# Optimization experiments

Hardware: AMD Instinct MI355X
Metric: run time of the kernel (lower is better)

Reference implementation:

```python
import jax, jax.numpy as jnp
import numpy as np

N = 50000       # nodes
E = 800000      # directed edges (avg degree 16)
DIN, DH, DOUT = 128, 128, 64
NUM_LAYERS = 5


def setup_inputs() -> dict:
    key = jax.random.key(0)
    ks = jax.random.split(key, 2 + 2 * NUM_LAYERS)
    x = jax.random.normal(ks[0], (N, DIN), dtype=jnp.float32)
    edge_index = jax.random.randint(ks[1], (2, E), 0, N, dtype=jnp.int64)
    dims = [(DIN, DH)] + [(DH, DH)] * (NUM_LAYERS - 2) + [(DH, DOUT)]
    inp = {"x": x, "edge_index": edge_index}
    for i, (di, do) in enumerate(dims):
        # PyG Linear weight is [out, in]; glorot-ish scale
        inp[f"W{i}"] = jax.random.normal(ks[2 + 2 * i], (do, di), dtype=jnp.float32) / np.sqrt(di)
        inp[f"b{i}"] = jnp.zeros((do,), dtype=jnp.float32)
    return inp


def gcn_conv(x, W, b, src, dst, n):
    """PyG GCNConv: symmetric normalization with self-loops (already appended)."""
    h = x @ W.T                                   # [N, do]
    ones = jnp.ones(src.shape[0], dtype=h.dtype)
    deg = jax.ops.segment_sum(ones, dst, num_segments=n)          # [N]
    dinv = jnp.where(deg > 0, jax.lax.rsqrt(jnp.maximum(deg, 1.0)), 0.0)
    norm = dinv[src] * dinv[dst]                  # [E+N]
    msg = h[src] * norm[:, None]                  # [E+N, do] gather
    out = jax.ops.segment_sum(msg, dst, num_segments=n)           # scatter-add
    return out + b


def reference(x, edge_index, W0, b0, W1, b1, W2, b2, W3, b3, W4, b4):
    n = x.shape[0]
    loop = jnp.arange(n, dtype=edge_index.dtype)
    src = jnp.concatenate([edge_index[0], loop])  # add self-loops
    dst = jnp.concatenate([edge_index[1], loop])
    Ws = [W0, W1, W2, W3, W4]
    bs = [b0, b1, b2, b3, b4]
    for i in range(NUM_LAYERS):
        x = gcn_conv(x, Ws[i], bs[i], src, dst, n)
        if i != NUM_LAYERS - 1:
            x = jax.nn.relu(x)
            # dropout is identity in eval mode (training=False)
    return x
```

## Files before the change

kernel.cpp:

```cpp
#include <hip/hip_runtime.h>
#include <hip/hip_fp16.h>
#include <math.h>


typedef _Float16 f16x8 __attribute__((ext_vector_type(8)));
typedef float f32x4 __attribute__((ext_vector_type(4)));

#define NBIN 128
#define NB 512
#define WCAP 12288


__device__ __forceinline__ int edge_at(const void* ei, int is64, long long idx) {
  if (is64) return (int)((const long long*)ei)[idx];
  return ((const int*)ei)[idx];
}

__device__ __forceinline__ int detect_is64(const int* ei32, int E, int* ldsflag, int tid) {
  if (tid == 0) *ldsflag = 0;
  __syncthreads();
  int lim = (E < 256) ? E : 256;
  if (tid < lim) {
    if (ei32[2 * tid + 1] != 0) atomicOr(ldsflag, 1);
  }
  __syncthreads();
  return (*ldsflag == 0) ? 1 : 0;
}

__global__ __launch_bounds__(512) void k_cnt2(const void* __restrict__ ei, int* __restrict__ bcnt,
                                              int E, int n, int W) {
  __shared__ int cnt[NBIN];
  __shared__ int f64;
  int t = threadIdx.x;
  int is64 = detect_is64((const int*)ei, E, &f64, t);
  if (t < NBIN) cnt[t] = 0;
  __syncthreads();
  int chunk = (E + NB - 1) / NB;
  int base = blockIdx.x * chunk;
  int end = base + chunk;
  if (end > E) end = E;
  for (int i = base + t; i < end; i += 512) {
    int s = edge_at(ei, is64, i);
    int v = edge_at(ei, is64, (long long)E + i);
    if ((unsigned)v < (unsigned)n && (unsigned)s < (unsigned)n) atomicAdd(&cnt[v / W], 1);
  }
  __syncthreads();
  if (t < NBIN) bcnt[blockIdx.x * NBIN + t] = cnt[t];
}

__global__ __launch_bounds__(256) void k_scanb(int* __restrict__ bcnt, int* __restrict__ bintot) {
  __shared__ int buf[NB];
  int bin = blockIdx.x;
  int t = threadIdx.x;
  int a0 = bcnt[(size_t)t * NBIN + bin];
  int a1 = bcnt[(size_t)(t + 256) * NBIN + bin];
  buf[t] = a0;
  buf[t + 256] = a1;
  __syncthreads();
  for (int off = 1; off < NB; off <<= 1) {
    int x0 = (t >= off) ? buf[t - off] : 0;
    int x1 = (t + 256 >= off) ? buf[t + 256 - off] : 0;
    __syncthreads();
    buf[t] += x0;
    buf[t + 256] += x1;
    __syncthreads();
  }
  bcnt[(size_t)t * NBIN + bin] = buf[t] - a0;
  bcnt[(size_t)(t + 256) * NBIN + bin] = buf[t + 256] - a1;
  if (t == 255) bintot[bin] = buf[NB - 1];
}

__global__ __launch_bounds__(512) void k_scat(const void* __restrict__ ei, const int* __restrict__ bintot,
                                              const int* __restrict__ bcnt, uint2* __restrict__ ebin,
                                              int E, int n, int W) {
  __shared__ int f64;
  __shared__ int sb[NBIN];
  __shared__ int cur[NBIN];
  int t = threadIdx.x;
  int is64 = detect_is64((const int*)ei, E, &f64, t);
  if (t < NBIN) sb[t] = bintot[t];
  __syncthreads();
  for (int off = 1; off < NBIN; off <<= 1) {
    int x = 0;
    if (t < NBIN && t >= off) x = sb[t - off];
    __syncthreads();
    if (t < NBIN) sb[t] += x;
    __syncthreads();
  }
  if (t < NBIN) cur[t] = sb[t] - bintot[t] + bcnt[blockIdx.x * NBIN + t];
  __syncthreads();
  int chunk = (E + NB - 1) / NB;
  int base = blockIdx.x * chunk;
  int end = base + chunk;
  if (end > E) end = E;
  for (int i = base + t; i < end; i += 512) {
    int s = edge_at(ei, is64, i);
    int v = edge_at(ei, is64, (long long)E + i);
    if ((unsigned)v < (unsigned)n && (unsigned)s < (unsigned)n) {
      int pos = atomicAdd(&cur[v / W], 1);
      ebin[pos] = make_uint2((unsigned)s, (unsigned)v);
    }
  }
}

__global__ __launch_bounds__(256) void k_build(const uint2* __restrict__ ebin, const int* __restrict__ bintot,
                                               int* __restrict__ row_ptr, float* __restrict__ dinv,
                                               int* __restrict__ col, int n, int W) {
  __shared__ int hist[512];
  __shared__ int scanBuf[512];
  __shared__ int sb[NBIN];
  __shared__ unsigned int win[WCAP];
  int t = threadIdx.x;
  int b = blockIdx.x;
  if (t < NBIN) sb[t] = bintot[t];
  __syncthreads();
  for (int off = 1; off < NBIN; off <<= 1) {
    int x = 0;
    if (t < NBIN && t >= off) x = sb[t - off];
    __syncthreads();
    if (t < NBIN) sb[t] += x;
    __syncthreads();
  }
  int ebase = sb[b] - bintot[b];
  int ecnt = bintot[b];
  int etotal = sb[NBIN - 1];

  int v0 = b * W;
  int v1 = v0 + W;
  if (v1 > n) v1 = n;
  int nloc = v1 - v0;
  if (nloc <= 0) {
    if (b == NBIN - 1 && t == 0) row_ptr[n] = etotal;
    return;
  }

  for (int i = t; i < 512; i += 256) { hist[i] = 0; scanBuf[i] = 0; }
  __syncthreads();
  for (int j = t; j < ecnt; j += 256) {
    uint2 e = ebin[ebase + j];
    atomicAdd(&hist[(int)e.y - v0], 1);
  }
  __syncthreads();
  for (int i = t; i < nloc; i += 256) {
    scanBuf[i] = hist[i];
    dinv[v0 + i] = 1.0f / sqrtf((float)(hist[i] + 1));
  }
  __syncthreads();
  int i1 = t, i2 = t + 256;
  for (int off = 1; off < 512; off <<= 1) {
    int a = (i1 >= off) ? scanBuf[i1 - off] : 0;
    int c = (i2 >= off) ? scanBuf[i2 - off] : 0;
    __syncthreads();
    scanBuf[i1] += a;
    scanBuf[i2] += c;
    __syncthreads();
  }
  for (int i = t; i < nloc; i += 256) row_ptr[v0 + i] = ebase + scanBuf[i] - hist[i];
  if (b == NBIN - 1 && t == 0) row_ptr[n] = etotal;
  __syncthreads();
  for (int i = t; i < nloc; i += 256) hist[i] = scanBuf[i] - hist[i];
  __syncthreads();
  if (ecnt <= WCAP) {
    for (int j = t; j < ecnt; j += 256) {
      uint2 e = ebin[ebase + j];
      int pos = atomicAdd(&hist[(int)e.y - v0], 1);
      win[pos] = e.x;
    }
    __syncthreads();
    for (int j = t; j < ecnt; j += 256) col[ebase + j] = (int)win[j];
  } else {
    for (int j = t; j < ecnt; j += 256) {
      uint2 e = ebin[ebase + j];
      int pos = atomicAdd(&hist[(int)e.y - v0], 1);
      col[ebase + pos] = (int)e.x;
    }
  }
}


__global__ __launch_bounds__(256) void k_split_x(const float* __restrict__ X, unsigned int* __restrict__ Xh,
                                                 unsigned int* __restrict__ Xr, int n2) {
  int i = blockIdx.x * 256 + threadIdx.x;
  if (i >= n2) return;
  float2 v = ((const float2*)X)[i];
  __half hx = __float2half(v.x), hy = __float2half(v.y);
  float rx = v.x - __half2float(hx), ry = v.y - __half2float(hy);
  __half rxh = __float2half(rx), ryh = __float2half(ry);
  Xh[i] = ((unsigned int)*(unsigned short*)&hy << 16) | *(unsigned short*)&hx;
  Xr[i] = ((unsigned int)*(unsigned short*)&ryh << 16) | *(unsigned short*)&rxh;
}

__global__ __launch_bounds__(256) void k_split_wall(const float* __restrict__ W0, const float* __restrict__ W1,
                                                    const float* __restrict__ W2, const float* __restrict__ W3,
                                                    const float* __restrict__ W4, unsigned short* __restrict__ Wh,
                                                    unsigned short* __restrict__ Wr, int total) {
  int i = blockIdx.x * 256 + threadIdx.x;
  if (i >= total) return;
  const float* src;
  int off;
  if (i < 65536) {
    int l = i >> 14;
    off = i & 16383;
    src = (l == 0) ? W0 : (l == 1) ? W1 : (l == 2) ? W2 : W3;
  } else {
    off = i - 65536;
    src = W4;
  }
  float v = src[off];
  __half h = __float2half(v);
  float r = v - __half2float(h);
  __half rh = __float2half(r);
  Wh[i] = *(unsigned short*)&h;
  Wr[i] = *(unsigned short*)&rh;
}


template <int DO>
__global__ __launch_bounds__(256) void gemm_mfma(const unsigned short* __restrict__ Xh,
                                                 const unsigned short* __restrict__ Xr,
                                                 const unsigned short* __restrict__ Wh,
                                                 const unsigned short* __restrict__ Wr,
                                                 const float* __restrict__ dinv, __half* __restrict__ G, int n) {
  constexpr int NCG = DO / 16;
  __shared__ unsigned short sWh[DO * 128];
  __shared__ unsigned short sWr[DO * 128];
  const int tid = threadIdx.x;

#pragma unroll
  for (int it = 0; it < DO / 16; ++it) {
    int t = it * 256 + tid;
    int row = t >> 4, ch = t & 15;
    int sch = ch ^ (row & 7);
    const uint4* gh = (const uint4*)&Wh[(size_t)t * 8];
    const uint4* gr = (const uint4*)&Wr[(size_t)t * 8];
    *(uint4*)&sWh[row * 128 + sch * 8] = *gh;
    *(uint4*)&sWr[row * 128 + sch * 8] = *gr;
  }

  const int wv = tid >> 6;
  const int l = tid & 63;
  const int m = l & 15;
  const int ks = l >> 4;
  const int gr0 = blockIdx.x * 64 + wv * 16;
  const int arow = gr0 + m;

  f16x8 ah[4], ar[4];
  const f16x8 z8 = {0, 0, 0, 0, 0, 0, 0, 0};
#pragma unroll
  for (int kb = 0; kb < 4; ++kb) {
    int koff = kb * 32 + ks * 8;
    if (arow < n) {
      ah[kb] = *(const f16x8*)&Xh[(size_t)arow * 128 + koff];
      ar[kb] = *(const f16x8*)&Xr[(size_t)arow * 128 + koff];
    } else {
      ah[kb] = z8;
      ar[kb] = z8;
    }
  }

  f32x4 acc[NCG];
#pragma unroll
  for (int c = 0; c < NCG; ++c) acc[c] = {0.f, 0.f, 0.f, 0.f};

  __syncthreads();

#pragma unroll
  for (int kb = 0; kb < 4; ++kb) {
    int ch = (kb * 4 + ks) ^ (m & 7);
#pragma unroll
    for (int c = 0; c < NCG; ++c) {
      int brow = c * 16 + m;
      f16x8 bh = *(const f16x8*)&sWh[brow * 128 + ch * 8];
      f16x8 br = *(const f16x8*)&sWr[brow * 128 + ch * 8];
      acc[c] = __builtin_amdgcn_mfma_f32_16x16x32_f16(ah[kb], bh, acc[c], 0, 0, 0);
      acc[c] = __builtin_amdgcn_mfma_f32_16x16x32_f16(ah[kb], br, acc[c], 0, 0, 0);
      acc[c] = __builtin_amdgcn_mfma_f32_16x16x32_f16(ar[kb], bh, acc[c], 0, 0, 0);
    }
  }

  int r0 = gr0 + ks * 4;
  float dv[4];
#pragma unroll
  for (int i = 0; i < 4; ++i) dv[i] = (r0 + i < n) ? dinv[r0 + i] : 0.f;
#pragma unroll
  for (int c = 0; c < NCG; ++c) {
#pragma unroll
    for (int i = 0; i < 4; ++i) {
      int row = r0 + i;
      if (row < n) G[(size_t)row * DO + c * 16 + m] = __float2half(dv[i] * acc[c][i]);
    }
  }
}


__device__ __forceinline__ float2 h2f(unsigned int u) {
  __half2 h = *(__half2*)&u;
  return __half22float2(h);
}

__global__ __launch_bounds__(256) void aggregate128(const unsigned int* __restrict__ G, const float* __restrict__ dinv,
                                                    const float* __restrict__ bias, const int* __restrict__ rp,
                                                    const int* __restrict__ col, unsigned int* __restrict__ Yh,
                                                    unsigned int* __restrict__ Yr, int n) {
  int v = (int)((blockIdx.x * 256 + threadIdx.x) >> 6);
  int lane = threadIdx.x & 63;
  if (v >= n) return;
  int s = rp[v], e = rp[v + 1];
  float2 a0 = h2f(G[(size_t)v * 64 + lane]);
  float2 a1 = make_float2(0.f, 0.f), a2 = make_float2(0.f, 0.f), a3 = make_float2(0.f, 0.f);
  float2 a4 = make_float2(0.f, 0.f), a5 = make_float2(0.f, 0.f);
  float2 a6 = make_float2(0.f, 0.f), a7 = make_float2(0.f, 0.f);
  int t = s;
  while (t < e) {
    int batch = e - t;
    if (batch > 64) batch = 64;
    int ci = col[t + (lane < batch ? lane : batch - 1)];
    int j = 0;
    for (; j + 8 <= batch; j += 8) {
      int u0 = __shfl(ci, j, 64), u1 = __shfl(ci, j + 1, 64);
      int u2 = __shfl(ci, j + 2, 64), u3 = __shfl(ci, j + 3, 64);
      int u4 = __shfl(ci, j + 4, 64), u5 = __shfl(ci, j + 5, 64);
      int u6 = __shfl(ci, j + 6, 64), u7 = __shfl(ci, j + 7, 64);
      unsigned int g0 = G[(size_t)u0 * 64 + lane];
      unsigned int g1 = G[(size_t)u1 * 64 + lane];
      unsigned int g2 = G[(size_t)u2 * 64 + lane];
      unsigned int g3 = G[(size_t)u3 * 64 + lane];
      unsigned int g4 = G[(size_t)u4 * 64 + lane];
      unsigned int g5 = G[(size_t)u5 * 64 + lane];
      unsigned int g6 = G[(size_t)u6 * 64 + lane];
      unsigned int g7 = G[(size_t)u7 * 64 + lane];
      float2 f0 = h2f(g0), f1 = h2f(g1), f2 = h2f(g2), f3 = h2f(g3);
      float2 f4 = h2f(g4), f5 = h2f(g5), f6 = h2f(g6), f7 = h2f(g7);
      a0.x += f0.x; a0.y += f0.y;
      a1.x += f1.x; a1.y += f1.y;
      a2.x += f2.x; a2.y += f2.y;
      a3.x += f3.x; a3.y += f3.y;
      a4.x += f4.x; a4.y += f4.y;
      a5.x += f5.x; a5.y += f5.y;
      a6.x += f6.x; a6.y += f6.y;
      a7.x += f7.x; a7.y += f7.y;
    }
    for (; j < batch; ++j) {
      int u = __shfl(ci, j, 64);
      float2 f = h2f(G[(size_t)u * 64 + lane]);
      a0.x += f.x; a0.y += f.y;
    }
    t += batch;
  }
  float sx = ((a0.x + a1.x) + (a2.x + a3.x)) + ((a4.x + a5.x) + (a6.x + a7.x));
  float sy = ((a0.y + a1.y) + (a2.y + a3.y)) + ((a4.y + a5.y) + (a6.y + a7.y));
  float dv = dinv[v];
  float2 bb = ((const float2*)bias)[lane];
  float ox = fmaxf(fmaf(dv, sx, bb.x), 0.f);
  float oy = fmaxf(fmaf(dv, sy, bb.y), 0.f);
  __half hx = __float2half(ox), hy = __float2half(oy);
  float rx = ox - __half2float(hx), ry = oy - __half2float(hy);
  __half rxh = __float2half(rx), ryh = __float2half(ry);
  size_t o = (size_t)v * 64 + lane;
  Yh[o] = ((unsigned int)*(unsigned short*)&hy << 16) | *(unsigned short*)&hx;
  Yr[o] = ((unsigned int)*(unsigned short*)&ryh << 16) | *(unsigned short*)&rxh;
}

__global__ __launch_bounds__(256) void aggregate64(const unsigned short* __restrict__ G, const float* __restrict__ dinv,
                                                   const float* __restrict__ bias, const int* __restrict__ rp,
                                                   const int* __restrict__ col, float* __restrict__ Y, int n) {
  int v = (int)((blockIdx.x * 256 + threadIdx.x) >> 6);
  int lane = threadIdx.x & 63;
  if (v >= n) return;
  int s = rp[v], e = rp[v + 1];
  float a0 = __half2float(*(const __half*)&G[(size_t)v * 64 + lane]);
  float a1 = 0.f, a2 = 0.f, a3 = 0.f;
  float a4 = 0.f, a5 = 0.f, a6 = 0.f, a7 = 0.f;
  int t = s;
  while (t < e) {
    int batch = e - t;
    if (batch > 64) batch = 64;
    int ci = col[t + (lane < batch ? lane : batch - 1)];
    int j = 0;
    for (; j + 8 <= batch; j += 8) {
      int u0 = __shfl(ci, j, 64), u1 = __shfl(ci, j + 1, 64);
      int u2 = __shfl(ci, j + 2, 64), u3 = __shfl(ci, j + 3, 64);
      int u4 = __shfl(ci, j + 4, 64), u5 = __shfl(ci, j + 5, 64);
      int u6 = __shfl(ci, j + 6, 64), u7 = __shfl(ci, j + 7, 64);
      unsigned short g0 = G[(size_t)u0 * 64 + lane];
      unsigned short g1 = G[(size_t)u1 * 64 + lane];
      unsigned short g2 = G[(size_t)u2 * 64 + lane];
      unsigned short g3 = G[(size_t)u3 * 64 + lane];
      unsigned short g4 = G[(size_t)u4 * 64 + lane];
      unsigned short g5 = G[(size_t)u5 * 64 + lane];
      unsigned short g6 = G[(size_t)u6 * 64 + lane];
      unsigned short g7 = G[(size_t)u7 * 64 + lane];
      a0 += __half2float(*(const __half*)&g0);
      a1 += __half2float(*(const __half*)&g1);
      a2 += __half2float(*(const __half*)&g2);
      a3 += __half2float(*(const __half*)&g3);
      a4 += __half2float(*(const __half*)&g4);
      a5 += __half2float(*(const __half*)&g5);
      a6 += __half2float(*(const __half*)&g6);
      a7 += __half2float(*(const __half*)&g7);
    }
    for (; j < batch; ++j) {
      int u = __shfl(ci, j, 64);
      unsigned short g = G[(size_t)u * 64 + lane];
      a0 += __half2float(*(const __half*)&g);
    }
    t += batch;
  }
  float sum = ((a0 + a1) + (a2 + a3)) + ((a4 + a5) + (a6 + a7));
  Y[(size_t)v * 64 + lane] = fmaf(dinv[v], sum, bias[lane]);
}


extern "C" void kernel_launch(void* const* d_in, const int* in_sizes, int n_in,
                              void* d_out, int out_size, void* d_ws, size_t ws_size,
                              hipStream_t stream) {
  const float* x = (const float*)d_in[0];
  const void* ei = d_in[1];
  const int N = in_sizes[0] / 128;
  const int E = in_sizes[1] / 2;
  const float* W[5] = {(const float*)d_in[2], (const float*)d_in[4], (const float*)d_in[6],
                       (const float*)d_in[8], (const float*)d_in[10]};
  const float* B[5] = {(const float*)d_in[3], (const float*)d_in[5], (const float*)d_in[7],
                       (const float*)d_in[9], (const float*)d_in[11]};
  const int Wbin = (N + NBIN - 1) / NBIN;

  char* p = (char*)d_ws;
  unsigned short* xyh = (unsigned short*)p;  p += (size_t)N * 128 * 2;
  unsigned short* xyr = (unsigned short*)p;  p += (size_t)N * 128 * 2;
  __half* g = (__half*)p;                    p += (size_t)N * 128 * 2;
  uint2* ebin = (uint2*)g;
  unsigned short* wh = (unsigned short*)p;   p += (size_t)5 * 16384 * 2;
  unsigned short* wr = (unsigned short*)p;   p += (size_t)5 * 16384 * 2;
  float* dinv = (float*)p;                   p += (size_t)N * 4;
  int* col = (int*)p;                        p += (size_t)E * 4;
  int* row_ptr = (int*)p;                    p += (size_t)(N + 1) * 4;
  int* bcnt = (int*)p;                       p += (size_t)NB * NBIN * 4;
  int* bintot = (int*)p;                     p += NBIN * 4;

  k_cnt2<<<NB, 512, 0, stream>>>(ei, bcnt, E, N, Wbin);
  k_scanb<<<NBIN, 256, 0, stream>>>(bcnt, bintot);
  k_scat<<<NB, 512, 0, stream>>>(ei, bintot, bcnt, ebin, E, N, Wbin);
  k_build<<<NBIN, 256, 0, stream>>>(ebin, bintot, row_ptr, dinv, col, N, Wbin);

  k_split_x<<<(N * 64 + 255) / 256, 256, 0, stream>>>(x, (unsigned int*)xyh, (unsigned int*)xyr, N * 64);
  k_split_wall<<<(73728 + 255) / 256, 256, 0, stream>>>(W[0], W[1], W[2], W[3], W[4], wh, wr, 73728);

  const int gb = (N + 63) / 64;
  const int ab = (N * 64 + 255) / 256;

  for (int l = 0; l < 4; ++l) {
    gemm_mfma<128><<<gb, 256, 0, stream>>>(xyh, xyr, wh + l * 16384, wr + l * 16384, dinv, g, N);
    aggregate128<<<ab, 256, 0, stream>>>((const unsigned int*)g, dinv, B[l], row_ptr, col,
                                         (unsigned int*)xyh, (unsigned int*)xyr, N);
  }
  gemm_mfma<64><<<gb, 256, 0, stream>>>(xyh, xyr, wh + 4 * 16384, wr + 4 * 16384, dinv, g, N);
  aggregate64<<<ab, 256, 0, stream>>>((const unsigned short*)g, dinv, B[4], row_ptr, col, (float*)d_out, N);
}
```

Baseline: 303.2 us.

## Fuse neighbor aggregation with next layer's MFMA GEMM via LDS staging

Replaces the separate aggregate128 and gemm_mfma launches for the middle layers with one kernel. A block aggregates 64 nodes into split fp16 hi/lo tiles held in LDS, then multiplies them by the next layer's weights with MFMA and writes the scaled result to a ping-pong buffer. This is meant to remove the global write and re-read of the intermediate activations and cut the number of launches. In exchange the aggregation runs only 4 waves per block over 16 rows each, with LDS pressure that may limit occupancy and latency hiding for the gathers.

```diff
diff --git a/kernel.cpp b/kernel.cpp
--- a/kernel.cpp
+++ b/kernel.cpp
@@ -9,6 +9,7 @@
 #define NBIN 128
 #define NB 512
 #define WCAP 12288
+#define SXW 136
 
 
 __device__ __forceinline__ int edge_at(const void* ei, int is64, long long idx) {
@@ -298,68 +299,132 @@
   return __half22float2(h);
 }
 
-__global__ __launch_bounds__(256) void aggregate128(const unsigned int* __restrict__ G, const float* __restrict__ dinv,
-                                                    const float* __restrict__ bias, const int* __restrict__ rp,
-                                                    const int* __restrict__ col, unsigned int* __restrict__ Yh,
-                                                    unsigned int* __restrict__ Yr, int n) {
-  int v = (int)((blockIdx.x * 256 + threadIdx.x) >> 6);
-  int lane = threadIdx.x & 63;
-  if (v >= n) return;
-  int s = rp[v], e = rp[v + 1];
-  float2 a0 = h2f(G[(size_t)v * 64 + lane]);
-  float2 a1 = make_float2(0.f, 0.f), a2 = make_float2(0.f, 0.f), a3 = make_float2(0.f, 0.f);
-  float2 a4 = make_float2(0.f, 0.f), a5 = make_float2(0.f, 0.f);
-  float2 a6 = make_float2(0.f, 0.f), a7 = make_float2(0.f, 0.f);
-  int t = s;
-  while (t < e) {
-    int batch = e - t;
-    if (batch > 64) batch = 64;
-    int ci = col[t + (lane < batch ? lane : batch - 1)];
-    int j = 0;
-    for (; j + 8 <= batch; j += 8) {
-      int u0 = __shfl(ci, j, 64), u1 = __shfl(ci, j + 1, 64);
-      int u2 = __shfl(ci, j + 2, 64), u3 = __shfl(ci, j + 3, 64);
-      int u4 = __shfl(ci, j + 4, 64), u5 = __shfl(ci, j + 5, 64);
-      int u6 = __shfl(ci, j + 6, 64), u7 = __shfl(ci, j + 7, 64);
-      unsigned int g0 = G[(size_t)u0 * 64 + lane];
-      unsigned int g1 = G[(size_t)u1 * 64 + lane];
-      unsigned int g2 = G[(size_t)u2 * 64 + lane];
-      unsigned int g3 = G[(size_t)u3 * 64 + lane];
-      unsigned int g4 = G[(size_t)u4 * 64 + lane];
-      unsigned int g5 = G[(size_t)u5 * 64 + lane];
-      unsigned int g6 = G[(size_t)u6 * 64 + lane];
-      unsigned int g7 = G[(size_t)u7 * 64 + lane];
-      float2 f0 = h2f(g0), f1 = h2f(g1), f2 = h2f(g2), f3 = h2f(g3);
-      float2 f4 = h2f(g4), f5 = h2f(g5), f6 = h2f(g6), f7 = h2f(g7);
-      a0.x += f0.x; a0.y += f0.y;
-      a1.x += f1.x; a1.y += f1.y;
-      a2.x += f2.x; a2.y += f2.y;
-      a3.x += f3.x; a3.y += f3.y;
-      a4.x += f4.x; a4.y += f4.y;
-      a5.x += f5.x; a5.y += f5.y;
-      a6.x += f6.x; a6.y += f6.y;
-      a7.x += f7.x; a7.y += f7.y;
-    }
-    for (; j < batch; ++j) {
-      int u = __shfl(ci, j, 64);
-      float2 f = h2f(G[(size_t)u * 64 + lane]);
-      a0.x += f.x; a0.y += f.y;
-    }
-    t += batch;
-  }
-  float sx = ((a0.x + a1.x) + (a2.x + a3.x)) + ((a4.x + a5.x) + (a6.x + a7.x));
-  float sy = ((a0.y + a1.y) + (a2.y + a3.y)) + ((a4.y + a5.y) + (a6.y + a7.y));
-  float dv = dinv[v];
-  float2 bb = ((const float2*)bias)[lane];
-  float ox = fmaxf(fmaf(dv, sx, bb.x), 0.f);
-  float oy = fmaxf(fmaf(dv, sy, bb.y), 0.f);
-  __half hx = __float2half(ox), hy = __float2half(oy);
-  float rx = ox - __half2float(hx), ry = oy - __half2float(hy);
-  __half rxh = __float2half(rx), ryh = __float2half(ry);
-  size_t o = (size_t)v * 64 + lane;
-  Yh[o] = ((unsigned int)*(unsigned short*)&hy << 16) | *(unsigned short*)&hx;
-  Yr[o] = ((unsigned int)*(unsigned short*)&ryh << 16) | *(unsigned short*)&rxh;
-}
+template <int DO>
+__global__ __launch_bounds__(256, 4) void fused_ag(const unsigned int* __restrict__ Gin,
+                                                   const float* __restrict__ dinv,
+                                                   const float* __restrict__ bias,
+                                                   const int* __restrict__ rp, const int* __restrict__ col,
+                                                   const unsigned short* __restrict__ Wh,
+                                                   const unsigned short* __restrict__ Wr,
+                                                   __half* __restrict__ Gout, int n) {
+  constexpr int NCG = DO / 16;
+  __shared__ unsigned short sXh[64 * SXW];
+  __shared__ unsigned short sXr[64 * SXW];
+
+  const int tid = threadIdx.x;
+  const int wv = tid >> 6, lane = tid & 63;
+  const int node0 = blockIdx.x * 64;
+
+  for (int k = 0; k < 16; ++k) {
+    int row = wv * 16 + k;
+    int v = node0 + row;
+    unsigned int ph = 0, pr = 0;
+    if (v < n) {
+      int s = rp[v], e = rp[v + 1];
+      float2 a0 = h2f(Gin[(size_t)v * 64 + lane]);
+      float2 a1 = make_float2(0.f, 0.f), a2 = make_float2(0.f, 0.f), a3 = make_float2(0.f, 0.f);
+      float2 a4 = make_float2(0.f, 0.f), a5 = make_float2(0.f, 0.f);
+      float2 a6 = make_float2(0.f, 0.f), a7 = make_float2(0.f, 0.f);
+      int t = s;
+      while (t < e) {
+        int batch = e - t;
+        if (batch > 64) batch = 64;
+        int ci = col[t + (lane < batch ? lane : batch - 1)];
+        int j = 0;
+        for (; j + 8 <= batch; j += 8) {
+          int u0 = __shfl(ci, j, 64), u1 = __shfl(ci, j + 1, 64);
+          int u2 = __shfl(ci, j + 2, 64), u3 = __shfl(ci, j + 3, 64);
+          int u4 = __shfl(ci, j + 4, 64), u5 = __shfl(ci, j + 5, 64);
+          int u6 = __shfl(ci, j + 6, 64), u7 = __shfl(ci, j + 7, 64);
+          unsigned int g0 = Gin[(size_t)u0 * 64 + lane];
+          unsigned int g1 = Gin[(size_t)u1 * 64 + lane];
+          unsigned int g2 = Gin[(size_t)u2 * 64 + lane];
+          unsigned int g3 = Gin[(size_t)u3 * 64 + lane];
+          unsigned int g4 = Gin[(size_t)u4 * 64 + lane];
+          unsigned int g5 = Gin[(size_t)u5 * 64 + lane];
+          unsigned int g6 = Gin[(size_t)u6 * 64 + lane];
+          unsigned int g7 = Gin[(size_t)u7 * 64 + lane];
+          float2 f0 = h2f(g0), f1 = h2f(g1), f2 = h2f(g2), f3 = h2f(g3);
+          float2 f4 = h2f(g4), f5 = h2f(g5), f6 = h2f(g6), f7 = h2f(g7);
+          a0.x += f0.x; a0.y += f0.y;
+          a1.x += f1.x; a1.y += f1.y;
+          a2.x += f2.x; a2.y += f2.y;
+          a3.x += f3.x; a3.y += f3.y;
+          a4.x += f4.x; a4.y += f4.y;
+          a5.x += f5.x; a5.y += f5.y;
+          a6.x += f6.x; a6.y += f6.y;
+          a7.x += f7.x; a7.y += f7.y;
+        }
+        for (; j < batch; ++j) {
+          int u = __shfl(ci, j, 64);
+          float2 f = h2f(Gin[(size_t)u * 64 + lane]);
+          a0.x += f.x; a0.y += f.y;
+        }
+        t += batch;
+      }
+      float sx = ((a0.x + a1.x) + (a2.x + a3.x)) + ((a4.x + a5.x) + (a6.x + a7.x));
+      float sy = ((a0.y + a1.y) + (a2.y + a3.y)) + ((a4.y + a5.y) + (a6.y + a7.y));
+      float dv = dinv[v];
+      float2 bb = ((const float2*)bias)[lane];
+      float ox = fmaxf(fmaf(dv, sx, bb.x), 0.f);
+      float oy = fmaxf(fmaf(dv, sy, bb.y), 0.f);
+      __half hx = __float2half(ox), hy = __float2half(oy);
+      float rx = ox - __half2float(hx), ry = oy - __half2float(hy);
+      __half rxh = __float2half(rx), ryh = __float2half(ry);
+      ph = ((unsigned int)*(unsigned short*)&hy << 16) | *(unsigned short*)&hx;
+      pr = ((unsigned int)*(unsigned short*)&ryh << 16) | *(unsigned short*)&rxh;
+    }
+    *(unsigned int*)&sXh[row * SXW + 2 * lane] = ph;
+    *(unsigned int*)&sXr[row * SXW + 2 * lane] = pr;
+  }
+  __syncthreads();
+
+  const int m = lane & 15;
+  const int ks = lane >> 4;
+  const int arow = wv * 16 + m;
+
+  f16x8 ah[4], ar[4];
+#pragma unroll
+  for (int kb = 0; kb < 4; ++kb) {
+    ah[kb] = *(const f16x8*)&sXh[arow * SXW + kb * 32 + ks * 8];
+    ar[kb] = *(const f16x8*)&sXr[arow * SXW + kb * 32 + ks * 8];
+  }
+
+  f32x4 acc[NCG];
+#pragma unroll
+  for (int c = 0; c < NCG; ++c) acc[c] = {0.f, 0.f, 0.f, 0.f};
+
+#pragma unroll
+  for (int c = 0; c < NCG; ++c) {
+    int brow = c * 16 + m;
+    f16x8 bh[4], br[4];
+#pragma unroll
+    for (int kb = 0; kb < 4; ++kb) {
+      bh[kb] = *(const f16x8*)&Wh[(size_t)brow * 128 + kb * 32 + ks * 8];
+      br[kb] = *(const f16x8*)&Wr[(size_t)brow * 128 + kb * 32 + ks * 8];
+    }
+#pragma unroll
+    for (int kb = 0; kb < 4; ++kb) {
+      acc[c] = __builtin_amdgcn_mfma_f32_16x16x32_f16(ah[kb], bh[kb], acc[c], 0, 0, 0);
+      acc[c] = __builtin_amdgcn_mfma_f32_16x16x32_f16(ah[kb], br[kb], acc[c], 0, 0, 0);
+      acc[c] = __builtin_amdgcn_mfma_f32_16x16x32_f16(ar[kb], bh[kb], acc[c], 0, 0, 0);
+    }
+  }
+
+  int r0 = node0 + wv * 16 + ks * 4;
+  float dv4[4];
+#pragma unroll
+  for (int i = 0; i < 4; ++i) dv4[i] = (r0 + i < n) ? dinv[r0 + i] : 0.f;
+#pragma unroll
+  for (int c = 0; c < NCG; ++c) {
+#pragma unroll
+    for (int i = 0; i < 4; ++i) {
+      int row = r0 + i;
+      if (row < n) Gout[(size_t)row * DO + c * 16 + m] = __float2half(dv4[i] * acc[c][i]);
+    }
+  }
+}
+
 
 __global__ __launch_bounds__(256) void aggregate64(const unsigned short* __restrict__ G, const float* __restrict__ dinv,
                                                    const float* __restrict__ bias, const int* __restrict__ rp,
@@ -427,8 +492,9 @@
   char* p = (char*)d_ws;
   unsigned short* xyh = (unsigned short*)p;  p += (size_t)N * 128 * 2;
   unsigned short* xyr = (unsigned short*)p;  p += (size_t)N * 128 * 2;
-  __half* g = (__half*)p;                    p += (size_t)N * 128 * 2;
-  uint2* ebin = (uint2*)g;
+  __half* ga = (__half*)p;                   p += (size_t)N * 128 * 2;
+  __half* gb = (__half*)p;                   p += (size_t)N * 128 * 2;
+  uint2* ebin = (uint2*)ga;
   unsigned short* wh = (unsigned short*)p;   p += (size_t)5 * 16384 * 2;
   unsigned short* wr = (unsigned short*)p;   p += (size_t)5 * 16384 * 2;
   float* dinv = (float*)p;                   p += (size_t)N * 4;
@@ -445,14 +511,17 @@
   k_split_x<<<(N * 64 + 255) / 256, 256, 0, stream>>>(x, (unsigned int*)xyh, (unsigned int*)xyr, N * 64);
   k_split_wall<<<(73728 + 255) / 256, 256, 0, stream>>>(W[0], W[1], W[2], W[3], W[4], wh, wr, 73728);
 
-  const int gb = (N + 63) / 64;
+  const int gb64 = (N + 63) / 64;
   const int ab = (N * 64 + 255) / 256;
 
-  for (int l = 0; l < 4; ++l) {
-    gemm_mfma<128><<<gb, 256, 0, stream>>>(xyh, xyr, wh + l * 16384, wr + l * 16384, dinv, g, N);
-    aggregate128<<<ab, 256, 0, stream>>>((const unsigned int*)g, dinv, B[l], row_ptr, col,
-                                         (unsigned int*)xyh, (unsigned int*)xyr, N);
-  }
-  gemm_mfma<64><<<gb, 256, 0, stream>>>(xyh, xyr, wh + 4 * 16384, wr + 4 * 16384, dinv, g, N);
-  aggregate64<<<ab, 256, 0, stream>>>((const unsigned short*)g, dinv, B[4], row_ptr, col, (float*)d_out, N);
-}
+  gemm_mfma<128><<<gb64, 256, 0, stream>>>(xyh, xyr, wh, wr, dinv, ga, N);
+  fused_ag<128><<<gb64, 256, 0, stream>>>((const unsigned int*)ga, dinv, B[0], row_ptr, col,
+                                          wh + 1 * 16384, wr + 1 * 16384, gb, N);
+  fused_ag<128><<<gb64, 256, 0, stream>>>((const unsigned int*)gb, dinv, B[1], row_ptr, col,
+                                          wh + 2 * 16384, wr + 2 * 16384, ga, N);
+  fused_ag<128><<<gb64, 256, 0, stream>>>((const unsigned int*)ga, dinv, B[2], row_ptr, col,
+                                          wh + 3 * 16384, wr + 3 * 16384, gb, N);
+  fused_ag<64><<<gb64, 256, 0, stream>>>((const unsigned int*)gb, dinv, B[3], row_ptr, col,
+                                         wh + 4 * 16384, wr + 4 * 16384, ga, N);
+  aggregate64<<<ab, 256, 0, stream>>>((const unsigned short*)ga, dinv, B[4], row_ptr, col, (float*)d_out, N);
+}
```

Result: slower. 422.6 us (+39.4%).

## Chunk hidden features by column and pin chunks to XCCs in aggregation

Applied to the files above, without the earlier changes.

The GEMM now writes the 128-wide fp16 hidden output as four column chunks of 32 halves per node. A new persistent aggregation kernel picks a chunk from the XCC id register and pulls tiles through per-chunk atomic counters, so each die mostly gathers from one chunk that fits in its own L2. The intent is better cache locality for the random neighbour gathers on a multi-die GPU. In exchange it adds atomic work-stealing, 16-lane groups with shorter gather batches, and depends on the hardware XCC id register.

```diff
diff --git a/kernel.cpp b/kernel.cpp
--- a/kernel.cpp
+++ b/kernel.cpp
@@ -9,6 +9,7 @@
 #define NBIN 128
 #define NB 512
 #define WCAP 12288
+#define GETREG_XCC_ID 63508
 
 
 __device__ __forceinline__ int edge_at(const void* ei, int is64, long long idx) {
@@ -215,7 +216,7 @@
 }
 
 
-template <int DO>
+template <int DO, bool CHUNKED>
 __global__ __launch_bounds__(256) void gemm_mfma(const unsigned short* __restrict__ Xh,
                                                  const unsigned short* __restrict__ Xr,
                                                  const unsigned short* __restrict__ Wh,
@@ -287,7 +288,15 @@
 #pragma unroll
     for (int i = 0; i < 4; ++i) {
       int row = r0 + i;
-      if (row < n) G[(size_t)row * DO + c * 16 + m] = __float2half(dv[i] * acc[c][i]);
+      if (row < n) {
+        __half val = __float2half(dv[i] * acc[c][i]);
+        if (CHUNKED) {
+          int j = c * 16 + m;
+          G[(size_t)(j >> 5) * ((size_t)n * 32) + (size_t)row * 32 + (j & 31)] = val;
+        } else {
+          G[(size_t)row * DO + c * 16 + m] = val;
+        }
+      }
     }
   }
 }
@@ -298,68 +307,82 @@
   return __half22float2(h);
 }
 
-__global__ __launch_bounds__(256) void aggregate128(const unsigned int* __restrict__ G, const float* __restrict__ dinv,
-                                                    const float* __restrict__ bias, const int* __restrict__ rp,
-                                                    const int* __restrict__ col, unsigned int* __restrict__ Yh,
-                                                    unsigned int* __restrict__ Yr, int n) {
-  int v = (int)((blockIdx.x * 256 + threadIdx.x) >> 6);
-  int lane = threadIdx.x & 63;
-  if (v >= n) return;
-  int s = rp[v], e = rp[v + 1];
-  float2 a0 = h2f(G[(size_t)v * 64 + lane]);
-  float2 a1 = make_float2(0.f, 0.f), a2 = make_float2(0.f, 0.f), a3 = make_float2(0.f, 0.f);
-  float2 a4 = make_float2(0.f, 0.f), a5 = make_float2(0.f, 0.f);
-  float2 a6 = make_float2(0.f, 0.f), a7 = make_float2(0.f, 0.f);
-  int t = s;
-  while (t < e) {
-    int batch = e - t;
-    if (batch > 64) batch = 64;
-    int ci = col[t + (lane < batch ? lane : batch - 1)];
-    int j = 0;
-    for (; j + 8 <= batch; j += 8) {
-      int u0 = __shfl(ci, j, 64), u1 = __shfl(ci, j + 1, 64);
-      int u2 = __shfl(ci, j + 2, 64), u3 = __shfl(ci, j + 3, 64);
-      int u4 = __shfl(ci, j + 4, 64), u5 = __shfl(ci, j + 5, 64);
-      int u6 = __shfl(ci, j + 6, 64), u7 = __shfl(ci, j + 7, 64);
-      unsigned int g0 = G[(size_t)u0 * 64 + lane];
-      unsigned int g1 = G[(size_t)u1 * 64 + lane];
-      unsigned int g2 = G[(size_t)u2 * 64 + lane];
-      unsigned int g3 = G[(size_t)u3 * 64 + lane];
-      unsigned int g4 = G[(size_t)u4 * 64 + lane];
-      unsigned int g5 = G[(size_t)u5 * 64 + lane];
-      unsigned int g6 = G[(size_t)u6 * 64 + lane];
-      unsigned int g7 = G[(size_t)u7 * 64 + lane];
-      float2 f0 = h2f(g0), f1 = h2f(g1), f2 = h2f(g2), f3 = h2f(g3);
-      float2 f4 = h2f(g4), f5 = h2f(g5), f6 = h2f(g6), f7 = h2f(g7);
-      a0.x += f0.x; a0.y += f0.y;
-      a1.x += f1.x; a1.y += f1.y;
-      a2.x += f2.x; a2.y += f2.y;
-      a3.x += f3.x; a3.y += f3.y;
-      a4.x += f4.x; a4.y += f4.y;
-      a5.x += f5.x; a5.y += f5.y;
-      a6.x += f6.x; a6.y += f6.y;
-      a7.x += f7.x; a7.y += f7.y;
-    }
-    for (; j < batch; ++j) {
-      int u = __shfl(ci, j, 64);
-      float2 f = h2f(G[(size_t)u * 64 + lane]);
-      a0.x += f.x; a0.y += f.y;
-    }
-    t += batch;
-  }
-  float sx = ((a0.x + a1.x) + (a2.x + a3.x)) + ((a4.x + a5.x) + (a6.x + a7.x));
-  float sy = ((a0.y + a1.y) + (a2.y + a3.y)) + ((a4.y + a5.y) + (a6.y + a7.y));
-  float dv = dinv[v];
-  float2 bb = ((const float2*)bias)[lane];
-  float ox = fmaxf(fmaf(dv, sx, bb.x), 0.f);
-  float oy = fmaxf(fmaf(dv, sy, bb.y), 0.f);
-  __half hx = __float2half(ox), hy = __float2half(oy);
-  float rx = ox - __half2float(hx), ry = oy - __half2float(hy);
-  __half rxh = __float2half(rx), ryh = __float2half(ry);
-  size_t o = (size_t)v * 64 + lane;
-  Yh[o] = ((unsigned int)*(unsigned short*)&hy << 16) | *(unsigned short*)&hx;
-  Yr[o] = ((unsigned int)*(unsigned short*)&ryh << 16) | *(unsigned short*)&rxh;
-}
+__global__ __launch_bounds__(256) void k_agg_chunk(const unsigned int* __restrict__ Gc,
+                                                   const float* __restrict__ dinv,
+                                                   const float* __restrict__ bias,
+                                                   const int* __restrict__ rp, const int* __restrict__ col,
+                                                   unsigned int* __restrict__ Yh, unsigned int* __restrict__ Yr,
+                                                   int* __restrict__ cur, int n, int ntiles) {
+  __shared__ int stile;
+  const int tid = threadIdx.x;
+  const int xcc = __builtin_amdgcn_s_getreg(GETREG_XCC_ID) & 15;
+  const int mychunk = xcc & 3;
+  const int grpid = tid >> 4;
+  const int r = tid & 15;
+  const int grpbase = (tid & 63) & 48;
+
+  for (int pass = 0; pass < 4; ++pass) {
+    int chunk = (mychunk + pass) & 3;
+    const unsigned int* gcb = Gc + (size_t)chunk * ((size_t)n * 16);
+    const float2* bias2 = (const float2*)bias + chunk * 16;
+    while (true) {
+      if (tid == 0) stile = atomicAdd(&cur[chunk], 1);
+      __syncthreads();
+      int tile = stile;
+      __syncthreads();
+      if (tile >= ntiles) break;
+#pragma unroll
+      for (int it = 0; it < 4; ++it) {
+        int v = tile * 64 + it * 16 + grpid;
+        if (v >= n) continue;
+        int s = rp[v], e = rp[v + 1];
+        float2 a0 = h2f(gcb[(size_t)v * 16 + r]);
+        float2 a1 = make_float2(0.f, 0.f), a2 = make_float2(0.f, 0.f), a3 = make_float2(0.f, 0.f);
+        int t = s;
+        while (t < e) {
+          int rem = e - t;
+          if (rem > 16) rem = 16;
+          int ci = col[t + (r < rem ? r : rem - 1)];
+          int j = 0;
+          for (; j + 4 <= rem; j += 4) {
+            int u0 = __shfl(ci, grpbase + j, 64);
+            int u1 = __shfl(ci, grpbase + j + 1, 64);
+            int u2 = __shfl(ci, grpbase + j + 2, 64);
+            int u3 = __shfl(ci, grpbase + j + 3, 64);
+            unsigned int g0 = gcb[(size_t)u0 * 16 + r];
+            unsigned int g1 = gcb[(size_t)u1 * 16 + r];
+            unsigned int g2 = gcb[(size_t)u2 * 16 + r];
+            unsigned int g3 = gcb[(size_t)u3 * 16 + r];
+            float2 f0 = h2f(g0), f1 = h2f(g1), f2 = h2f(g2), f3 = h2f(g3);
+            a0.x += f0.x; a0.y += f0.y;
+            a1.x += f1.x; a1.y += f1.y;
+            a2.x += f2.x; a2.y += f2.y;
+            a3.x += f3.x; a3.y += f3.y;
+          }
+          for (; j < rem; ++j) {
+            int u = __shfl(ci, grpbase + j, 64);
+            float2 f = h2f(gcb[(size_t)u * 16 + r]);
+            a0.x += f.x; a0.y += f.y;
+          }
+          t += rem;
+        }
+        float sx = (a0.x + a1.x) + (a2.x + a3.x);
+        float sy = (a0.y + a1.y) + (a2.y + a3.y);
+        float dv = dinv[v];
+        float2 bb = bias2[r];
+        float ox = fmaxf(fmaf(dv, sx, bb.x), 0.f);
+        float oy = fmaxf(fmaf(dv, sy, bb.y), 0.f);
+        __half hx = __float2half(ox), hy = __float2half(oy);
+        float rx = ox - __half2float(hx), ry = oy - __half2float(hy);
+        __half rxh = __float2half(rx), ryh = __float2half(ry);
+        size_t o = (size_t)v * 64 + chunk * 16 + r;
+        Yh[o] = ((unsigned int)*(unsigned short*)&hy << 16) | *(unsigned short*)&hx;
+        Yr[o] = ((unsigned int)*(unsigned short*)&ryh << 16) | *(unsigned short*)&rxh;
+      }
+    }
+  }
+}
+
 
 __global__ __launch_bounds__(256) void aggregate64(const unsigned short* __restrict__ G, const float* __restrict__ dinv,
                                                    const float* __restrict__ bias, const int* __restrict__ rp,
@@ -436,6 +459,9 @@
   int* row_ptr = (int*)p;                    p += (size_t)(N + 1) * 4;
   int* bcnt = (int*)p;                       p += (size_t)NB * NBIN * 4;
   int* bintot = (int*)p;                     p += NBIN * 4;
+  int* cur = (int*)p;                        p += 16 * 4;
+
+  hipMemsetAsync(cur, 0, 16 * sizeof(int), stream);
 
   k_cnt2<<<NB, 512, 0, stream>>>(ei, bcnt, E, N, Wbin);
   k_scanb<<<NBIN, 256, 0, stream>>>(bcnt, bintot);
@@ -445,14 +471,15 @@
   k_split_x<<<(N * 64 + 255) / 256, 256, 0, stream>>>(x, (unsigned int*)xyh, (unsigned int*)xyr, N * 64);
   k_split_wall<<<(73728 + 255) / 256, 256, 0, stream>>>(W[0], W[1], W[2], W[3], W[4], wh, wr, 73728);
 
-  const int gb = (N + 63) / 64;
+  const int gb64 = (N + 63) / 64;
   const int ab = (N * 64 + 255) / 256;
+  const int ntiles = (N + 63) / 64;
 
   for (int l = 0; l < 4; ++l) {
-    gemm_mfma<128><<<gb, 256, 0, stream>>>(xyh, xyr, wh + l * 16384, wr + l * 16384, dinv, g, N);
-    aggregate128<<<ab, 256, 0, stream>>>((const unsigned int*)g, dinv, B[l], row_ptr, col,
-                                         (unsigned int*)xyh, (unsigned int*)xyr, N);
-  }
-  gemm_mfma<64><<<gb, 256, 0, stream>>>(xyh, xyr, wh + 4 * 16384, wr + 4 * 16384, dinv, g, N);
+    gemm_mfma<128, true><<<gb64, 256, 0, stream>>>(xyh, xyr, wh + l * 16384, wr + l * 16384, dinv, g, N);
+    k_agg_chunk<<<2048, 256, 0, stream>>>((const unsigned int*)g, dinv, B[l], row_ptr, col,
+                                          (unsigned int*)xyh, (unsigned int*)xyr, cur + l * 4, N, ntiles);
+  }
+  gemm_mfma<64, false><<<gb64, 256, 0, stream>>>(xyh, xyr, wh + 4 * 16384, wr + 4 * 16384, dinv, g, N);
   aggregate64<<<ab, 256, 0, stream>>>((const unsigned short*)g, dinv, B[4], row_ptr, col, (float*)d_out, N);
 }
```

After: 740.8 us. 144% more time.
